# Kernel optimization log

Hardware: AMD Instinct MI355X
Metric: run time of the kernel (lower is better)

The kernel has to match this reference:

```python
import jax, jax.numpy as jnp
import numpy as np

N_NODES = 100000
N_EDGES = 3200000


def _sage_conv(x, src, dst, Wl, Wr, b):
    # PyG SAGEConv (aggr='mean', root_weight=True, bias on lin_l):
    # out_i = mean_{j in N(i)} x_j @ Wl + x_i @ Wr + b
    msg = x[src]                                            # [E, F] gather
    s = jax.ops.segment_sum(msg, dst, num_segments=N_NODES)  # [N, F]
    cnt = jax.ops.segment_sum(jnp.ones((src.shape[0], 1), x.dtype), dst,
                              num_segments=N_NODES)          # [N, 1]
    agg = s / jnp.maximum(cnt, 1.0)                          # mean (0 for isolated nodes)
    return agg @ Wl + x @ Wr + b


def setup_inputs() -> dict:
    key = jax.random.key(0)
    ks = jax.random.split(key, 12)
    in_d, hid, out_d = 32, 24, 12
    x = jax.random.normal(ks[0], (N_NODES, in_d), dtype=jnp.float32)
    edge_index = jax.random.randint(ks[1], (2, N_EDGES), 0, N_NODES, dtype=jnp.int64)

    def glorot(k, fan_in, fan_out):
        lim = np.sqrt(6.0 / (fan_in + fan_out)).astype(np.float32)
        return jax.random.uniform(k, (fan_in, fan_out), jnp.float32, -lim, lim)

    return {
        "x": x,
        "edge_index": edge_index,
        "Wl1": glorot(ks[2], in_d, hid), "Wr1": glorot(ks[3], in_d, hid),
        "b1": jnp.zeros((hid,), jnp.float32),
        "Wl2": glorot(ks[4], hid, hid), "Wr2": glorot(ks[5], hid, hid),
        "b2": jnp.zeros((hid,), jnp.float32),
        "Wl3": glorot(ks[6], hid, out_d), "Wr3": glorot(ks[7], hid, out_d),
        "b3": jnp.zeros((out_d,), jnp.float32),
    }


def reference(x, edge_index, Wl1, Wr1, b1, Wl2, Wr2, b2, Wl3, Wr3, b3):
    src, dst = edge_index[0], edge_index[1]
    h = jax.nn.relu(_sage_conv(x, src, dst, Wl1, Wr1, b1))
    h = jax.nn.relu(_sage_conv(h, src, dst, Wl2, Wr2, b2))
    h = jax.nn.sigmoid(_sage_conv(h, src, dst, Wl3, Wr3, b3))
    return h
```

## Files before the change

kernel.cpp:

```cpp
#include <hip/hip_runtime.h>
#include <cstdint>
#include <cstddef>

#define NT 256
constexpr int SHIFT  = 7;
constexpr int NBK    = 1024;
constexpr int BMASK  = (1 << SHIFT) - 1;
constexpr int EPB    = 6400;
constexpr int NPR    = 512;
constexpr int TSPLIT = 50000;
constexpr int STCAP  = 6144;

__device__ __forceinline__ float sigf(float v) {
    return 1.0f / (1.0f + __expf(-v));
}
__device__ __forceinline__ float bf2f(unsigned short u) {
    return __uint_as_float((unsigned)u << 16);
}
__device__ __forceinline__ unsigned short f2bf(float f) {
    unsigned u = __float_as_uint(f);
    return (unsigned short)((u + 0x7fffu + ((u >> 16) & 1u)) >> 16);
}

__global__ __launch_bounds__(NT)
void part_k(const int* __restrict__ src, const int* __restrict__ dst,
            unsigned* __restrict__ part, int* __restrict__ runcntT,
            int* __restrict__ runstartT, int e_total, int nPB)
{
    __shared__ unsigned stage[EPB];
    __shared__ int hist[NBK];
    __shared__ int curs[NBK];
    __shared__ int tsum[NT];
    const int b    = blockIdx.x;
    const int t    = threadIdx.x;
    const int base = b * EPB;
    const int nh   = min(EPB, e_total - base);

    for (int i = t; i < NBK; i += NT) hist[i] = 0;
    __syncthreads();
    for (int i = t; i < nh; i += NT)
        atomicAdd(&hist[dst[base + i] >> SHIFT], 1);
    __syncthreads();

    for (int i = t; i < NBK; i += NT)
        runcntT[(size_t)b * NBK + i] = hist[i];

    const int f0 = 4 * t;
    int h0 = hist[f0], h1 = hist[f0 + 1], h2 = hist[f0 + 2], h3 = hist[f0 + 3];
    int incl = h0 + h1 + h2 + h3;
    tsum[t] = incl;
    __syncthreads();
    for (int off = 1; off < NT; off <<= 1) {
        int add = (t >= off) ? tsum[t - off] : 0;
        __syncthreads();
        tsum[t] += add;
        __syncthreads();
    }
    int ex = tsum[t] - incl;
    curs[f0]     = ex;
    curs[f0 + 1] = ex + h0;
    curs[f0 + 2] = ex + h0 + h1;
    curs[f0 + 3] = ex + h0 + h1 + h2;
    int* rsp = &runstartT[(size_t)b * NBK + f0];
    rsp[0] = base + ex;
    rsp[1] = base + ex + h0;
    rsp[2] = base + ex + h0 + h1;
    rsp[3] = base + ex + h0 + h1 + h2;
    __syncthreads();

    for (int i = t; i < nh; i += NT) {
        int d = dst[base + i];
        int s = src[base + i];
        int f = d >> SHIFT;
        int r = atomicAdd(&curs[f], 1);
        stage[r] = ((unsigned)s << SHIFT) | (unsigned)(d & BMASK);
    }
    __syncthreads();

    for (int i = t; i < nh; i += NT) part[base + i] = stage[i];
}

__global__ __launch_bounds__(NT)
void csum_k(const int* __restrict__ runcntT, int* __restrict__ totcnt, int nPB)
{
    __shared__ int sm[8][33];
    const int c  = threadIdx.x & 31;
    const int r0 = threadIdx.x >> 5;
    const int f0 = blockIdx.x * 32;
    int acc = 0;
    for (int r = r0; r < nPB; r += 8)
        acc += runcntT[(size_t)r * NBK + f0 + c];
    sm[r0][c] = acc;
    __syncthreads();
    if (threadIdx.x < 32) {
        int s = 0;
#pragma unroll
        for (int i = 0; i < 8; ++i) s += sm[i][threadIdx.x];
        totcnt[f0 + threadIdx.x] = s;
    }
}

__global__ __launch_bounds__(1024)
void tscan_k(const int* __restrict__ totcnt, int* __restrict__ fbase)
{
    __shared__ int s[1024];
    int t = threadIdx.x;
    int v = totcnt[t];
    s[t] = v;
    __syncthreads();
    for (int off = 1; off < 1024; off <<= 1) {
        int add = (t >= off) ? s[t - off] : 0;
        __syncthreads();
        s[t] += add;
        __syncthreads();
    }
    fbase[t] = s[t] - v;
}

__global__ __launch_bounds__(NT)
void xp2_k(const int* __restrict__ runcntT, const int* __restrict__ runstartT,
           int* __restrict__ runcntF, int* __restrict__ runstartF, int nPB)
{
    __shared__ int tc[32][33];
    __shared__ int ts[32][33];
    const int t  = threadIdx.x;
    const int fb = blockIdx.x & 31;
    const int bb = blockIdx.x >> 5;
    const int f0 = fb * 32;
    const int b0 = bb * 32;
    const int r  = t >> 5;
    const int c  = t & 31;

#pragma unroll
    for (int j = 0; j < 4; ++j) {
        int bi = r + 8 * j;
        int b = b0 + bi;
        if (b < nPB) {
            tc[bi][c] = runcntT [(size_t)b * NBK + f0 + c];
            ts[bi][c] = runstartT[(size_t)b * NBK + f0 + c];
        }
    }
    __syncthreads();
#pragma unroll
    for (int j = 0; j < 4; ++j) {
        int fi = r + 8 * j;
        int b = b0 + c;
        if (b < nPB) {
            runcntF [(size_t)(f0 + fi) * nPB + b] = tc[c][fi];
            runstartF[(size_t)(f0 + fi) * nPB + b] = ts[c][fi];
        }
    }
}

__global__ __launch_bounds__(NT)
void b_k(const unsigned* __restrict__ part, const int* __restrict__ runstartF,
         const int* __restrict__ runcntF, const int* __restrict__ fbase,
         int* __restrict__ row_ptr, int* __restrict__ mptr,
         int* __restrict__ col, int nPB, int n)
{
    constexpr int NB2 = 1 << SHIFT;
    __shared__ unsigned stage[STCAP];
    __shared__ int rss[NPR], rcs[NPR], lof[NPR];
    __shared__ int ssum[NT];
    __shared__ int d0[NB2], dt[NB2], sc[NB2], c0[NB2], c1[NB2];
    const int f = blockIdx.x;
    const int t = threadIdx.x;

    const int l0 = 2 * t, l1 = 2 * t + 1;
    int rc0 = (l0 < nPB) ? runcntF [(size_t)f * nPB + l0] : 0;
    int rc1 = (l1 < nPB) ? runcntF [(size_t)f * nPB + l1] : 0;
    rss[l0] = (l0 < nPB) ? runstartF[(size_t)f * nPB + l0] : 0;
    rss[l1] = (l1 < nPB) ? runstartF[(size_t)f * nPB + l1] : 0;
    rcs[l0] = rc0;
    rcs[l1] = rc1;
    int incl = rc0 + rc1;
    ssum[t] = incl;
    __syncthreads();
    for (int off = 1; off < NT; off <<= 1) {
        int add = (t >= off) ? ssum[t - off] : 0;
        __syncthreads();
        ssum[t] += add;
        __syncthreads();
    }
    int ex = ssum[t] - incl;
    lof[l0] = ex;
    lof[l1] = ex + rc0;
    __syncthreads();
    const int tot = ssum[NT - 1];

    if (t < NB2) { d0[t] = 0; dt[t] = 0; }
    __syncthreads();

    if (tot <= STCAP) {
        const int lane = t & 7;
        const int rg   = t >> 3;
        for (int chunk = 0; chunk < nPB; chunk += 32) {
            int r = chunk + rg;
            if (r < nPB) {
                int s0 = rss[r], c = rcs[r], lo = lof[r];
                for (int i = lane; i < c; i += 8)
                    stage[lo + i] = part[s0 + i];
            }
        }
        __syncthreads();
        for (int i = t; i < tot; i += NT) {
            unsigned p = stage[i];
            int l = p & BMASK;
            atomicAdd(&dt[l], 1);
            if ((int)(p >> SHIFT) < TSPLIT) atomicAdd(&d0[l], 1);
        }
    } else {
        for (int r = t; r < nPB; r += NT) {
            int s0 = rss[r], c = rcs[r];
            for (int i = 0; i < c; ++i) {
                unsigned p = part[s0 + i];
                int l = p & BMASK;
                atomicAdd(&dt[l], 1);
                if ((int)(p >> SHIFT) < TSPLIT) atomicAdd(&d0[l], 1);
            }
        }
    }
    __syncthreads();

    if (t < NB2) sc[t] = dt[t];
    __syncthreads();
    for (int off = 1; off < NB2; off <<= 1) {
        int add = (t >= off && t < NB2) ? sc[t - off] : 0;
        __syncthreads();
        if (t < NB2) sc[t] += add;
        __syncthreads();
    }
    if (t < NB2) {
        int excl = sc[t] - dt[t];
        int st0  = fbase[f] + excl;
        int node = (f << SHIFT) + t;
        if (node <= n) row_ptr[node] = st0;
        if (node <  n) mptr[node]    = st0 + d0[t];
        c0[t] = st0;
        c1[t] = st0 + d0[t];
    }
    __syncthreads();

    if (tot <= STCAP) {
        for (int i = t; i < tot; i += NT) {
            unsigned p = stage[i];
            int l = p & BMASK;
            int s = (int)(p >> SHIFT);
            int pos = atomicAdd((s < TSPLIT) ? &c0[l] : &c1[l], 1);
            col[pos] = s;
        }
    } else {
        for (int r = t; r < nPB; r += NT) {
            int s0 = rss[r], c = rcs[r];
            for (int i = 0; i < c; ++i) {
                unsigned p = part[s0 + i];
                int l = p & BMASK;
                int s = (int)(p >> SHIFT);
                int pos = atomicAdd((s < TSPLIT) ? &c0[l] : &c1[l], 1);
                col[pos] = s;
            }
        }
    }
}

__global__ __launch_bounds__(NT)
void cvt_k(const float* __restrict__ x, unsigned short* __restrict__ xb, int ntot)
{
    int i = blockIdx.x * NT + threadIdx.x;
    if (i < ntot) xb[i] = f2bf(x[i]);
}

__global__ __launch_bounds__(NT)
void gA_k(const unsigned short* __restrict__ Hin, const int* __restrict__ row_ptr,
          const int* __restrict__ mptr, const int* __restrict__ col,
          float* __restrict__ P, int n)
{
    const int lane8 = threadIdx.x & 7;
    const int grp   = threadIdx.x >> 3;
    const int node  = blockIdx.x * (NT / 8) + grp;
    if (node >= n) return;
    const int e0 = row_ptr[node];
    const int e1 = mptr[node];
    const ushort4* rows = reinterpret_cast<const ushort4*>(Hin);
    float a0 = 0.f, a1 = 0.f, a2 = 0.f, a3 = 0.f;
    int e = e0;
    for (; e + 3 < e1; e += 4) {
        int s0 = col[e], s1 = col[e + 1], s2 = col[e + 2], s3 = col[e + 3];
        ushort4 v0 = rows[(size_t)s0 * 8 + lane8];
        ushort4 v1 = rows[(size_t)s1 * 8 + lane8];
        ushort4 v2 = rows[(size_t)s2 * 8 + lane8];
        ushort4 v3 = rows[(size_t)s3 * 8 + lane8];
        a0 += bf2f(v0.x) + bf2f(v1.x) + bf2f(v2.x) + bf2f(v3.x);
        a1 += bf2f(v0.y) + bf2f(v1.y) + bf2f(v2.y) + bf2f(v3.y);
        a2 += bf2f(v0.z) + bf2f(v1.z) + bf2f(v2.z) + bf2f(v3.z);
        a3 += bf2f(v0.w) + bf2f(v1.w) + bf2f(v2.w) + bf2f(v3.w);
    }
    for (; e < e1; ++e) {
        ushort4 v0 = rows[(size_t)col[e] * 8 + lane8];
        a0 += bf2f(v0.x); a1 += bf2f(v0.y); a2 += bf2f(v0.z); a3 += bf2f(v0.w);
    }
    reinterpret_cast<float4*>(P + (size_t)node * 32)[lane8] = make_float4(a0, a1, a2, a3);
}

template<int FIN, int FOUT, int ACT>
__global__ __launch_bounds__(NT)
void gB_k(const unsigned short* __restrict__ Hin, const int* __restrict__ row_ptr,
          const int* __restrict__ mptr, const int* __restrict__ col,
          const float* __restrict__ P, const float* __restrict__ Wl,
          const float* __restrict__ Wr, const float* __restrict__ b,
          void* __restrict__ Hout, int n)
{
    constexpr int FS  = 32;
    constexpr int NPB = NT / 8;
    constexpr int GS  = 2 * FS + 4;
    __shared__ float sm[NPB * GS];

    const int lane8 = threadIdx.x & 7;
    const int grp   = threadIdx.x >> 3;
    const int node  = blockIdx.x * NPB + grp;
    const bool valid = node < n;

    if (valid) {
        const int rp0 = row_ptr[node];
        const int rpm = mptr[node];
        const int rp1 = row_ptr[node + 1];
        const ushort4* rows = reinterpret_cast<const ushort4*>(Hin);
        float4 pv = reinterpret_cast<const float4*>(P + (size_t)node * 32)[lane8];
        float a0 = pv.x, a1 = pv.y, a2 = pv.z, a3 = pv.w;
        ushort4 xv = rows[(size_t)node * 8 + lane8];
        int e = rpm;
        for (; e + 3 < rp1; e += 4) {
            int s0 = col[e], s1 = col[e + 1], s2 = col[e + 2], s3 = col[e + 3];
            ushort4 v0 = rows[(size_t)s0 * 8 + lane8];
            ushort4 v1 = rows[(size_t)s1 * 8 + lane8];
            ushort4 v2 = rows[(size_t)s2 * 8 + lane8];
            ushort4 v3 = rows[(size_t)s3 * 8 + lane8];
            a0 += bf2f(v0.x) + bf2f(v1.x) + bf2f(v2.x) + bf2f(v3.x);
            a1 += bf2f(v0.y) + bf2f(v1.y) + bf2f(v2.y) + bf2f(v3.y);
            a2 += bf2f(v0.z) + bf2f(v1.z) + bf2f(v2.z) + bf2f(v3.z);
            a3 += bf2f(v0.w) + bf2f(v1.w) + bf2f(v2.w) + bf2f(v3.w);
        }
        for (; e < rp1; ++e) {
            ushort4 v0 = rows[(size_t)col[e] * 8 + lane8];
            a0 += bf2f(v0.x); a1 += bf2f(v0.y); a2 += bf2f(v0.z); a3 += bf2f(v0.w);
        }
        float invd = 1.0f / fmaxf((float)(rp1 - rp0), 1.0f);
        float* smg = sm + grp * GS;
        smg[4 * lane8 + 0]      = a0 * invd;
        smg[4 * lane8 + 1]      = a1 * invd;
        smg[4 * lane8 + 2]      = a2 * invd;
        smg[4 * lane8 + 3]      = a3 * invd;
        smg[FS + 4 * lane8 + 0] = bf2f(xv.x);
        smg[FS + 4 * lane8 + 1] = bf2f(xv.y);
        smg[FS + 4 * lane8 + 2] = bf2f(xv.z);
        smg[FS + 4 * lane8 + 3] = bf2f(xv.w);
    }
    __syncthreads();

    if (!valid) return;
    const float* smg = sm + grp * GS;

    if constexpr (ACT == 0) {
        unsigned short* out = (unsigned short*)Hout + (size_t)node * FS;
#pragma unroll
        for (int j = 0; j < 4; ++j) {
            int f = lane8 + 8 * j;
            float r = 0.0f;
            if (f < FOUT) {
                float a = b[f];
#pragma unroll
                for (int k = 0; k < FIN; ++k) {
                    a = fmaf(smg[k],      Wl[k * FOUT + f], a);
                    a = fmaf(smg[FS + k], Wr[k * FOUT + f], a);
                }
                r = fmaxf(a, 0.0f);
            }
            out[f] = f2bf(r);
        }
    } else {
        float* out = (float*)Hout + (size_t)node * FOUT;
#pragma unroll
        for (int j = 0; j < (FOUT + 7) / 8; ++j) {
            int f = lane8 + 8 * j;
            if (f < FOUT) {
                float a = b[f];
#pragma unroll
                for (int k = 0; k < FIN; ++k) {
                    a = fmaf(smg[k],      Wl[k * FOUT + f], a);
                    a = fmaf(smg[FS + k], Wr[k * FOUT + f], a);
                }
                out[f] = sigf(a);
            }
        }
    }
}

extern "C" void kernel_launch(void* const* d_in, const int* in_sizes, int n_in,
                              void* d_out, int out_size, void* d_ws, size_t ws_size,
                              hipStream_t stream)
{
    const float* x   = (const float*)d_in[0];
    const int*   ei  = (const int*)d_in[1];
    const float* Wl1 = (const float*)d_in[2];
    const float* Wr1 = (const float*)d_in[3];
    const float* b1  = (const float*)d_in[4];
    const float* Wl2 = (const float*)d_in[5];
    const float* Wr2 = (const float*)d_in[6];
    const float* b2  = (const float*)d_in[7];
    const float* Wl3 = (const float*)d_in[8];
    const float* Wr3 = (const float*)d_in[9];
    const float* b3  = (const float*)d_in[10];

    const int N = in_sizes[0] / 32;
    const int E = in_sizes[1] / 2;
    const int* src = ei;
    const int* dst = ei + E;

    const int nPB = (E + EPB - 1) / EPB;
    const int nBK = ((N - 1) >> SHIFT) + 1;
    const int nbG = (N + 31) / 32;
    const int nbC = (N * 32 + NT - 1) / NT;
    const int nbX = 32 * ((nPB + 31) / 32);

    int* runstartT = (int*)d_ws;
    int* runcntT   = runstartT + (size_t)NBK * nPB;
    int* runstartF = runcntT + (size_t)NBK * nPB;
    int* runcntF   = runstartF + (size_t)NBK * nPB;
    int* totcnt    = runcntF + (size_t)NBK * nPB;
    int* fbase     = totcnt + 1024;
    int* row_ptr   = fbase + 1024;
    int* mptr      = row_ptr + (N + 2);
    size_t off     = 4 * (size_t)NBK * nPB + 2048 + (N + 2) + N;
    off = (off + 3) & ~(size_t)3;
    int* col       = (int*)d_ws + off;
    off += E;
    unsigned* part = (unsigned*)((int*)d_ws + off);
    float*    P    = (float*)part;
    off += E;
    unsigned short* xb  = (unsigned short*)((int*)d_ws + off);
    unsigned short* H1b = xb  + (size_t)N * 32;
    unsigned short* H2b = H1b + (size_t)N * 32;

    part_k <<<nPB, NT,   0, stream>>>(src, dst, part, runcntT, runstartT, E, nPB);
    csum_k <<<32,  NT,   0, stream>>>(runcntT, totcnt, nPB);
    tscan_k<<<1,   1024, 0, stream>>>(totcnt, fbase);
    xp2_k  <<<nbX, NT,   0, stream>>>(runcntT, runstartT, runcntF, runstartF, nPB);
    b_k    <<<nBK, NT,   0, stream>>>(part, runstartF, runcntF, fbase, row_ptr, mptr, col, nPB, N);

    cvt_k  <<<nbC, NT,   0, stream>>>(x, xb, N * 32);

    gA_k            <<<nbG, NT, 0, stream>>>(xb,  row_ptr, mptr, col, P, N);
    gB_k<32, 24, 0> <<<nbG, NT, 0, stream>>>(xb,  row_ptr, mptr, col, P, Wl1, Wr1, b1, H1b, N);
    gA_k            <<<nbG, NT, 0, stream>>>(H1b, row_ptr, mptr, col, P, N);
    gB_k<24, 24, 0> <<<nbG, NT, 0, stream>>>(H1b, row_ptr, mptr, col, P, Wl2, Wr2, b2, H2b, N);
    gA_k            <<<nbG, NT, 0, stream>>>(H2b, row_ptr, mptr, col, P, N);
    gB_k<24, 12, 1> <<<nbG, NT, 0, stream>>>(H2b, row_ptr, mptr, col, P, Wl3, Wr3, b3, (float*)d_out, N);
}
```

Baseline: 262.4 us.

## Sort nodes by in-degree within each bucket to balance gather warps

The CSR-build kernel now counting-sorts the nodes of each 128-node bucket by in-degree and writes a permutation array. The gather kernels process nodes in that permuted order, so the 8 node groups sharing a wavefront have similar edge counts and lanes idle less from divergent loop trip counts. This costs an extra perm load per node, less contiguous P and output writes, and some extra shared-memory scan work in b_k.

Result: slower. 285.6 us (+8.8%).

```diff
diff --git a/kernel.cpp b/kernel.cpp
--- a/kernel.cpp
+++ b/kernel.cpp
@@ -156,13 +156,14 @@
 void b_k(const unsigned* __restrict__ part, const int* __restrict__ runstartF,
          const int* __restrict__ runcntF, const int* __restrict__ fbase,
          int* __restrict__ row_ptr, int* __restrict__ mptr,
-         int* __restrict__ col, int nPB, int n)
+         int* __restrict__ col, int* __restrict__ perm, int nPB, int n)
 {
     constexpr int NB2 = 1 << SHIFT;
     __shared__ unsigned stage[STCAP];
     __shared__ int rss[NPR], rcs[NPR], lof[NPR];
     __shared__ int ssum[NT];
     __shared__ int d0[NB2], dt[NB2], sc[NB2], c0[NB2], c1[NB2];
+    __shared__ int dbin[64], dcur[64];
     const int f = blockIdx.x;
     const int t = threadIdx.x;
 
@@ -189,6 +190,7 @@
     const int tot = ssum[NT - 1];
 
     if (t < NB2) { d0[t] = 0; dt[t] = 0; }
+    if (t < 64) dbin[t] = 0;
     __syncthreads();
 
     if (tot <= STCAP) {
@@ -261,6 +263,24 @@
             }
         }
     }
+
+    const int node2 = (f << SHIFT) + t;
+    if (t < NB2 && node2 < n) atomicAdd(&dbin[min(dt[t], 63)], 1);
+    __syncthreads();
+    if (t < 64) ssum[t] = dbin[t];
+    __syncthreads();
+    for (int off = 1; off < 64; off <<= 1) {
+        int add = (t >= off && t < 64) ? ssum[t - off] : 0;
+        __syncthreads();
+        if (t < 64) ssum[t] += add;
+        __syncthreads();
+    }
+    if (t < 64) dcur[t] = ssum[t] - dbin[t];
+    __syncthreads();
+    if (t < NB2 && node2 < n) {
+        int r = atomicAdd(&dcur[min(dt[t], 63)], 1);
+        perm[(f << SHIFT) + r] = node2;
+    }
 }
 
 __global__ __launch_bounds__(NT)
@@ -273,12 +293,13 @@
 __global__ __launch_bounds__(NT)
 void gA_k(const unsigned short* __restrict__ Hin, const int* __restrict__ row_ptr,
           const int* __restrict__ mptr, const int* __restrict__ col,
-          float* __restrict__ P, int n)
+          const int* __restrict__ perm, float* __restrict__ P, int n)
 {
     const int lane8 = threadIdx.x & 7;
     const int grp   = threadIdx.x >> 3;
-    const int node  = blockIdx.x * (NT / 8) + grp;
-    if (node >= n) return;
+    const int gid   = blockIdx.x * (NT / 8) + grp;
+    if (gid >= n) return;
+    const int node  = perm[gid];
     const int e0 = row_ptr[node];
     const int e1 = mptr[node];
     const ushort4* rows = reinterpret_cast<const ushort4*>(Hin);
@@ -306,9 +327,9 @@
 __global__ __launch_bounds__(NT)
 void gB_k(const unsigned short* __restrict__ Hin, const int* __restrict__ row_ptr,
           const int* __restrict__ mptr, const int* __restrict__ col,
-          const float* __restrict__ P, const float* __restrict__ Wl,
-          const float* __restrict__ Wr, const float* __restrict__ b,
-          void* __restrict__ Hout, int n)
+          const int* __restrict__ perm, const float* __restrict__ P,
+          const float* __restrict__ Wl, const float* __restrict__ Wr,
+          const float* __restrict__ b, void* __restrict__ Hout, int n)
 {
     constexpr int FS  = 32;
     constexpr int NPB = NT / 8;
@@ -317,8 +338,9 @@
 
     const int lane8 = threadIdx.x & 7;
     const int grp   = threadIdx.x >> 3;
-    const int node  = blockIdx.x * NPB + grp;
-    const bool valid = node < n;
+    const int gid   = blockIdx.x * NPB + grp;
+    const bool valid = gid < n;
+    const int node  = valid ? perm[gid] : 0;
 
     if (valid) {
         const int rp0 = row_ptr[node];
@@ -359,6 +381,7 @@
 
     if (!valid) return;
     const float* smg = sm + grp * GS;
+    constexpr int OPL = (FOUT + 7) / 8;
 
     if constexpr (ACT == 0) {
         unsigned short* out = (unsigned short*)Hout + (size_t)node * FS;
@@ -380,7 +403,7 @@
     } else {
         float* out = (float*)Hout + (size_t)node * FOUT;
 #pragma unroll
-        for (int j = 0; j < (FOUT + 7) / 8; ++j) {
+        for (int j = 0; j < OPL; ++j) {
             int f = lane8 + 8 * j;
             if (f < FOUT) {
                 float a = b[f];
@@ -430,7 +453,8 @@
     int* fbase     = totcnt + 1024;
     int* row_ptr   = fbase + 1024;
     int* mptr      = row_ptr + (N + 2);
-    size_t off     = 4 * (size_t)NBK * nPB + 2048 + (N + 2) + N;
+    int* perm      = mptr + N;
+    size_t off     = 4 * (size_t)NBK * nPB + 2048 + (N + 2) + 2 * (size_t)N;
     off = (off + 3) & ~(size_t)3;
     int* col       = (int*)d_ws + off;
     off += E;
@@ -445,14 +469,14 @@
     csum_k <<<32,  NT,   0, stream>>>(runcntT, totcnt, nPB);
     tscan_k<<<1,   1024, 0, stream>>>(totcnt, fbase);
     xp2_k  <<<nbX, NT,   0, stream>>>(runcntT, runstartT, runcntF, runstartF, nPB);
-    b_k    <<<nBK, NT,   0, stream>>>(part, runstartF, runcntF, fbase, row_ptr, mptr, col, nPB, N);
+    b_k    <<<nBK, NT,   0, stream>>>(part, runstartF, runcntF, fbase, row_ptr, mptr, col, perm, nPB, N);
 
     cvt_k  <<<nbC, NT,   0, stream>>>(x, xb, N * 32);
 
-    gA_k            <<<nbG, NT, 0, stream>>>(xb,  row_ptr, mptr, col, P, N);
-    gB_k<32, 24, 0> <<<nbG, NT, 0, stream>>>(xb,  row_ptr, mptr, col, P, Wl1, Wr1, b1, H1b, N);
-    gA_k            <<<nbG, NT, 0, stream>>>(H1b, row_ptr, mptr, col, P, N);
-    gB_k<24, 24, 0> <<<nbG, NT, 0, stream>>>(H1b, row_ptr, mptr, col, P, Wl2, Wr2, b2, H2b, N);
-    gA_k            <<<nbG, NT, 0, stream>>>(H2b, row_ptr, mptr, col, P, N);
-    gB_k<24, 12, 1> <<<nbG, NT, 0, stream>>>(H2b, row_ptr, mptr, col, P, Wl3, Wr3, b3, (float*)d_out, N);
-}
+    gA_k            <<<nbG, NT, 0, stream>>>(xb,  row_ptr, mptr, col, perm, P, N);
+    gB_k<32, 24, 0> <<<nbG, NT, 0, stream>>>(xb,  row_ptr, mptr, col, perm, P, Wl1, Wr1, b1, H1b, N);
+    gA_k            <<<nbG, NT, 0, stream>>>(H1b, row_ptr, mptr, col, perm, P, N);
+    gB_k<24, 24, 0> <<<nbG, NT, 0, stream>>>(H1b, row_ptr, mptr, col, perm, P, Wl2, Wr2, b2, H2b, N);
+    gA_k            <<<nbG, NT, 0, stream>>>(H2b, row_ptr, mptr, col, perm, P, N);
+    gB_k<24, 12, 1> <<<nbG, NT, 0, stream>>>(H2b, row_ptr, mptr, col, perm, P, Wl3, Wr3, b3, (float*)d_out, N);
+}
```
